# Kernel optimization log

Hardware: AMD Instinct MI355X
Metric: run time of the kernel (lower is better)

The kernel has to match this reference:

```python
import jax, jax.numpy as jnp
import numpy as np


def setup_inputs() -> dict:
    key = jax.random.key(0)
    k1, k2, k3 = jax.random.split(key, 3)
    b_n, f_num, N = 2, 4, 50
    n = b_n * f_num
    C_in, C = 256, 64
    h, w = 200, 336
    return {
        "x": jax.random.normal(k1, (n, C, h * w), jnp.float32),
        "idx_feat": jax.random.normal(k2, (n, C_in, N, 1), jnp.float32),
        "weight": jax.random.normal(k3, (C, C_in), jnp.float32) * 0.01,
        "bias": jnp.zeros((C,), jnp.float32),
        "thing_gt_idx": jnp.ones((b_n, N, f_num), jnp.int32),
        "h": h,
        "w": w,
    }


def _con_loss(mw, b_n, N, f_num, C):
    # mw: (b_n*f_num, C, N, 1) kernel embeddings after embed_extractor
    K = N * f_num
    # reshape/permute mirrors torch: (b_n, N, f_num, C) flattened row-major ->
    # rows ordered (instance, frame), matching the boolean-mask gather order
    # under a dense (all-ones) thing_gt_idx mask.
    m = mw.reshape(b_n, f_num, C, N).transpose(0, 3, 1, 2).reshape(b_n, K, C)
    # F.normalize(dim=1)
    m = m / jnp.maximum(jnp.linalg.norm(m, axis=-1, keepdims=True), 1e-12)
    sim = jnp.einsum('bkc,blc->bkl', m, m)  # (b_n, K, K)
    labels = np.repeat(np.arange(N), f_num)  # instance id per row (static)
    f_own = np.tile(np.arange(f_num), N)     # frame id per row (static)
    # static negative gather indices: all columns of other instances, padded by
    # repeating the last negative (torch's while-loop torch.cat) to length K-1
    neg_cols = []
    for i in range(N):
        cols = np.nonzero(labels != i)[0]
        neg_cols.append(np.concatenate([cols, np.full(f_num - 1, cols[-1])]))
    neg_idx = np.stack(neg_cols)[labels]     # (K, K-1)
    # random positive among the f_num-1 same-instance / other-frame entries
    r = jax.random.randint(jax.random.key(42), (b_n, K), 0, f_num - 1)
    pos_off = jnp.where(r >= f_own[None, :], r + 1, r)
    pos_col = labels[None, :] * f_num + pos_off  # (b_n, K)
    positives = sim[jnp.arange(b_n)[:, None], jnp.arange(K)[None, :], pos_col]
    negatives = sim[:, np.arange(K)[:, None], neg_idx]  # (b_n, K, K-1)
    logits = jnp.concatenate([positives[..., None], negatives], axis=-1) / 0.07
    # CrossEntropyLoss with target 0, mean over K rows, summed over batches
    lse = jax.scipy.special.logsumexp(logits, axis=-1)
    return jnp.sum(jnp.mean(lse - logits[..., 0], axis=-1))


def reference(x, idx_feat, weight, bias, thing_gt_idx, h, w):
    b_n, N, f_num = thing_gt_idx.shape
    n = b_n * f_num
    C = weight.shape[0]
    # embed_extractor: 1x1 conv == channel matmul
    mw = jnp.einsum('bcnk,dc->bdnk', idx_feat, weight) + bias[None, :, None, None]
    loss = _con_loss(mw, b_n, N, f_num, C)
    # shuffle_times == 1 branch: kernels @ encoded features
    kernels = mw.reshape(n, C, N).transpose(0, 2, 1)  # (n, N, C)
    inst_pred = jnp.matmul(kernels, x).reshape(n, N, h, w)
    return inst_pred, loss
```

## Files before the change

kernel.cpp:

```cpp
#include <hip/hip_runtime.h>
#include <stdint.h>
#include <float.h>
#include <math.h>

#define HW_TOT 67200
#define NBF 8
#define CO 64
#define CI 256
#define NN 50
#define KK 200
#define BN 2

__device__ __forceinline__ uint32_t rotl32(uint32_t v, int n) {
  return (v << n) | (v >> (32 - n));
}

__device__ void tf2x32(uint32_t k0, uint32_t k1, uint32_t x0, uint32_t x1,
                       uint32_t& o0, uint32_t& o1) {
  const uint32_t ks2 = k0 ^ k1 ^ 0x1BD11BDAu;
  x0 += k0; x1 += k1;
  x0 += x1; x1 = rotl32(x1, 13); x1 ^= x0;
  x0 += x1; x1 = rotl32(x1, 15); x1 ^= x0;
  x0 += x1; x1 = rotl32(x1, 26); x1 ^= x0;
  x0 += x1; x1 = rotl32(x1, 6);  x1 ^= x0;
  x0 += k1; x1 += ks2 + 1u;
  x0 += x1; x1 = rotl32(x1, 17); x1 ^= x0;
  x0 += x1; x1 = rotl32(x1, 29); x1 ^= x0;
  x0 += x1; x1 = rotl32(x1, 16); x1 ^= x0;
  x0 += x1; x1 = rotl32(x1, 24); x1 ^= x0;
  x0 += ks2; x1 += k0 + 2u;
  x0 += x1; x1 = rotl32(x1, 13); x1 ^= x0;
  x0 += x1; x1 = rotl32(x1, 15); x1 ^= x0;
  x0 += x1; x1 = rotl32(x1, 26); x1 ^= x0;
  x0 += x1; x1 = rotl32(x1, 6);  x1 ^= x0;
  x0 += k0; x1 += k1 + 3u;
  x0 += x1; x1 = rotl32(x1, 17); x1 ^= x0;
  x0 += x1; x1 = rotl32(x1, 29); x1 ^= x0;
  x0 += x1; x1 = rotl32(x1, 16); x1 ^= x0;
  x0 += x1; x1 = rotl32(x1, 24); x1 ^= x0;
  x0 += k1; x1 += ks2 + 4u;
  x0 += x1; x1 = rotl32(x1, 13); x1 ^= x0;
  x0 += x1; x1 = rotl32(x1, 15); x1 ^= x0;
  x0 += x1; x1 = rotl32(x1, 26); x1 ^= x0;
  x0 += x1; x1 = rotl32(x1, 6);  x1 ^= x0;
  o0 = x0 + ks2;
  o1 = x1 + k0 + 5u;
}

__device__ int jax_r(int b, int k) {
  uint32_t k1a, k1b, k2a, k2b, h0, h1, l0, l1;
  tf2x32(0u, 42u, 0u, 0u, k1a, k1b);
  tf2x32(0u, 42u, 0u, 1u, k2a, k2b);
  const uint32_t idx = (uint32_t)(b * KK + k);
  tf2x32(k1a, k1b, 0u, idx, h0, h1);
  tf2x32(k2a, k2b, 0u, idx, l0, l1);
  const uint32_t hb = h0 ^ h1, lb = l0 ^ l1;
  return (int)(((hb % 3u) + (lb % 3u)) % 3u);
}

__global__ __launch_bounds__(256) void k_mw(const float* __restrict__ idx_feat,
                                            const float* __restrict__ weight,
                                            const float* __restrict__ bias,
                                            float* __restrict__ mw) {
  const int tid = blockIdx.x * 256 + threadIdx.x;
  if (tid >= NBF * CO * NN) return;
  const int n = tid % NN;
  const int rest = tid / NN;
  const int d = rest % CO;
  const int b = rest / CO;
  float acc = bias[d];
  const float* feat = idx_feat + (size_t)(b * CI) * NN + n;
  const float* wrow = weight + d * CI;
  #pragma unroll 8
  for (int ci = 0; ci < CI; ++ci)
    acc = fmaf(feat[ci * NN], wrow[ci], acc);
  mw[tid] = acc;
}

__device__ __forceinline__ float waveMax(float v) {
  #pragma unroll
  for (int o = 32; o > 0; o >>= 1) v = fmaxf(v, __shfl_down(v, o));
  return v;
}
__device__ __forceinline__ float waveSum(float v) {
  #pragma unroll
  for (int o = 32; o > 0; o >>= 1) v += __shfl_down(v, o);
  return v;
}

__global__ __launch_bounds__(256) void k_loss(const float* __restrict__ mw,
                                              float* __restrict__ partial) {
  __shared__ __align__(16) float m_lds[KK][68];
  __shared__ float red[8];
  __shared__ float pos_sh;
  __shared__ int rvals[32];

  const int b = blockIdx.x >> 3;
  const int chunk = blockIdx.x & 7;
  const int t = threadIdx.x;
  const int wid = t >> 6, lane = t & 63;
  const int kbase = chunk * 25;

  if (t < 25) rvals[t] = jax_r(b, kbase + t);

  float row[CO];
  if (t < KK) {
    const int f = t & 3, ni = t >> 2;
    const float* src = mw + (size_t)((b * 4 + f) * CO) * NN + ni;
    float ssq = 0.f;
    #pragma unroll
    for (int c = 0; c < CO; ++c) { const float v = src[c * NN]; row[c] = v; ssq += v * v; }
    const float inv = 1.0f / fmaxf(sqrtf(ssq), 1e-12f);
    #pragma unroll
    for (int c = 0; c < CO; ++c) { row[c] *= inv; m_lds[t][c] = row[c]; }
  }
  __syncthreads();

  float part = 0.f;
  for (int kk = 0; kk < 25; ++kk) {
    const int k = kbase + kk;
    const int g = k >> 2, fo = k & 3;
    const int r = rvals[kk];
    const int pos_off = (r >= fo) ? r + 1 : r;
    const int pos_col = (g << 2) + pos_off;
    const int last_neg = (g == NN - 1) ? (KK - 5) : (KK - 1);

    float dot = 0.f;
    if (t < KK) {
      const float4* mk = reinterpret_cast<const float4*>(&m_lds[k][0]);
      #pragma unroll
      for (int c4 = 0; c4 < 16; ++c4) {
        const float4 a = mk[c4];
        dot = fmaf(a.x, row[4 * c4 + 0], dot);
        dot = fmaf(a.y, row[4 * c4 + 1], dot);
        dot = fmaf(a.z, row[4 * c4 + 2], dot);
        dot = fmaf(a.w, row[4 * c4 + 3], dot);
      }
    }
    const float logit = dot * (1.0f / 0.07f);

    float wgt = 0.f;
    if (t < KK) {
      if (t == pos_col) wgt = 1.f;
      else if ((t >> 2) != g) wgt = (t == last_neg) ? 4.f : 1.f;
    }
    const bool valid = wgt > 0.f;

    const float wmax = waveMax(valid ? logit : -FLT_MAX);
    if (lane == 0) red[wid] = wmax;
    if (t == pos_col) pos_sh = logit;
    __syncthreads();
    const float mx = fmaxf(fmaxf(red[0], red[1]), fmaxf(red[2], red[3]));
    const float pos = pos_sh;
    const float ws = waveSum(valid ? wgt * expf(logit - mx) : 0.f);
    if (lane == 0) red[4 + wid] = ws;
    __syncthreads();
    if (t == 0) {
      const float s = red[4] + red[5] + red[6] + red[7];
      part += (mx + logf(s)) - pos;
    }
    __syncthreads();
  }
  if (t == 0) partial[blockIdx.x] = part;
}

typedef __attribute__((ext_vector_type(8))) short bf16x8;
typedef __attribute__((ext_vector_type(4))) float f32x4;

__device__ __forceinline__ uint32_t bf16rne(float f) {
  uint32_t u = __builtin_bit_cast(uint32_t, f);
  return (u + 0x7FFFu + ((u >> 16) & 1u)) >> 16;
}

__global__ __launch_bounds__(256, 4) void k_pred(const float* __restrict__ x,
                                                 const float* __restrict__ mw,
                                                 const float* __restrict__ partial,
                                                 float* __restrict__ out) {
  __shared__ __align__(16) char lds[64 * 128];

  const int b = blockIdx.y;
  const int p0 = blockIdx.x * 64;
  const int u = threadIdx.x;
  const int l = u & 63;
  const int w = u >> 6;
  const int ln = l & 15, lg = l >> 4;

  const float* xb  = x  + (size_t)b * CO * HW_TOT;
  const float* mwb = mw + (size_t)b * CO * NN;

  const int sc0 = 4 * (u >> 4);
  const int sp0 = 4 * (u & 15);
  const float4 v0 = *reinterpret_cast<const float4*>(xb + (size_t)(sc0 + 0) * HW_TOT + p0 + sp0);
  const float4 v1 = *reinterpret_cast<const float4*>(xb + (size_t)(sc0 + 1) * HW_TOT + p0 + sp0);
  const float4 v2 = *reinterpret_cast<const float4*>(xb + (size_t)(sc0 + 2) * HW_TOT + p0 + sp0);
  const float4 v3 = *reinterpret_cast<const float4*>(xb + (size_t)(sc0 + 3) * HW_TOT + p0 + sp0);

  bf16x8 afr[2];
  #pragma unroll
  for (int ks = 0; ks < 2; ++ks) {
    #pragma unroll
    for (int j = 0; j < 8; ++j) {
      const int c = ks * 32 + lg * 8 + j;
      const int n = min(16 * w + ln, NN - 1);
      afr[ks][j] = (short)bf16rne(mwb[c * NN + n]);
    }
  }

  {
    const float c0s[4] = {v0.x, v1.x, v2.x, v3.x};
    const float c1s[4] = {v0.y, v1.y, v2.y, v3.y};
    const float c2s[4] = {v0.z, v1.z, v2.z, v3.z};
    const float c3s[4] = {v0.w, v1.w, v2.w, v3.w};
    const float* cols[4] = {c0s, c1s, c2s, c3s};
    #pragma unroll
    for (int s = 0; s < 4; ++s) {
      const float* cv = cols[s];
      const uint32_t lo = bf16rne(cv[0]) | (bf16rne(cv[1]) << 16);
      const uint32_t hi = bf16rne(cv[2]) | (bf16rne(cv[3]) << 16);
      const int row = sp0 + s;
      const int wb = (row * 128 + sc0 * 2) ^ ((row & 7) << 4);
      *reinterpret_cast<uint2*>(lds + wb) = make_uint2(lo, hi);
    }
  }
  __syncthreads();

  f32x4 acc[4];
  #pragma unroll
  for (int q = 0; q < 4; ++q) acc[q] = (f32x4){0.f, 0.f, 0.f, 0.f};

  #pragma unroll
  for (int ks = 0; ks < 2; ++ks) {
    #pragma unroll
    for (int q = 0; q < 4; ++q) {
      const int row = q * 16 + ln;
      const int rb = (row * 128 + ks * 64 + lg * 16) ^ ((ln & 7) << 4);
      const uint4 raw = *reinterpret_cast<const uint4*>(lds + rb);
      const bf16x8 bfr = __builtin_bit_cast(bf16x8, raw);
      acc[q] = __builtin_amdgcn_mfma_f32_16x16x32_bf16(afr[ks], bfr, acc[q], 0, 0, 0);
    }
  }

  float* ob = out + (size_t)b * NN * HW_TOT + p0;
  #pragma unroll
  for (int q = 0; q < 4; ++q) {
    #pragma unroll
    for (int i = 0; i < 4; ++i) {
      const int n = 16 * w + 4 * lg + i;
      if (n < NN)
        __builtin_nontemporal_store(acc[q][i], ob + (size_t)n * HW_TOT + q * 16 + ln);
    }
  }

  if (blockIdx.x == 0 && b == 0 && u == 0) {
    float s = 0.f;
    #pragma unroll
    for (int i = 0; i < 16; ++i) s += partial[i];
    out[(size_t)NBF * NN * HW_TOT] = s * (1.0f / KK);
  }
}

extern "C" void kernel_launch(void* const* d_in, const int* in_sizes, int n_in,
                              void* d_out, int out_size, void* d_ws, size_t ws_size,
                              hipStream_t stream) {
  const float* x        = (const float*)d_in[0];
  const float* idx_feat = (const float*)d_in[1];
  const float* weight   = (const float*)d_in[2];
  const float* bias     = (const float*)d_in[3];
  float* out = (float*)d_out;

  float* mw = (float*)d_ws;
  float* partial = mw + NBF * CO * NN;

  hipLaunchKernelGGL(k_mw, dim3((NBF * CO * NN + 255) / 256), dim3(256), 0, stream,
                     idx_feat, weight, bias, mw);
  hipLaunchKernelGGL(k_loss, dim3(16), dim3(256), 0, stream, mw, partial);
  hipLaunchKernelGGL(k_pred, dim3(HW_TOT / 64, NBF), dim3(256), 0, stream,
                     x, mw, partial, out);
}
```

Baseline: 92.49 us.

## Process multiple pixel tiles per block with register prefetch of next tile

```diff
diff --git a/kernel.cpp b/kernel.cpp
--- a/kernel.cpp
+++ b/kernel.cpp
@@ -10,6 +10,7 @@
 #define NN 50
 #define KK 200
 #define BN 2
+#define TILES 5
 
 __device__ __forceinline__ uint32_t rotl32(uint32_t v, int n) {
   return (v << n) | (v >> (32 - n));
@@ -179,7 +180,6 @@
   __shared__ __align__(16) char lds[64 * 128];
 
   const int b = blockIdx.y;
-  const int p0 = blockIdx.x * 64;
   const int u = threadIdx.x;
   const int l = u & 63;
   const int w = u >> 6;
@@ -190,10 +190,7 @@
 
   const int sc0 = 4 * (u >> 4);
   const int sp0 = 4 * (u & 15);
-  const float4 v0 = *reinterpret_cast<const float4*>(xb + (size_t)(sc0 + 0) * HW_TOT + p0 + sp0);
-  const float4 v1 = *reinterpret_cast<const float4*>(xb + (size_t)(sc0 + 1) * HW_TOT + p0 + sp0);
-  const float4 v2 = *reinterpret_cast<const float4*>(xb + (size_t)(sc0 + 2) * HW_TOT + p0 + sp0);
-  const float4 v3 = *reinterpret_cast<const float4*>(xb + (size_t)(sc0 + 3) * HW_TOT + p0 + sp0);
+  const int pbase = blockIdx.x * (64 * TILES);
 
   bf16x8 afr[2];
   #pragma unroll
@@ -206,48 +203,71 @@
     }
   }
 
+  float4 v0, v1, v2, v3;
   {
-    const float c0s[4] = {v0.x, v1.x, v2.x, v3.x};
-    const float c1s[4] = {v0.y, v1.y, v2.y, v3.y};
-    const float c2s[4] = {v0.z, v1.z, v2.z, v3.z};
-    const float c3s[4] = {v0.w, v1.w, v2.w, v3.w};
-    const float* cols[4] = {c0s, c1s, c2s, c3s};
-    #pragma unroll
-    for (int s = 0; s < 4; ++s) {
-      const float* cv = cols[s];
-      const uint32_t lo = bf16rne(cv[0]) | (bf16rne(cv[1]) << 16);
-      const uint32_t hi = bf16rne(cv[2]) | (bf16rne(cv[3]) << 16);
-      const int row = sp0 + s;
-      const int wb = (row * 128 + sc0 * 2) ^ ((row & 7) << 4);
-      *reinterpret_cast<uint2*>(lds + wb) = make_uint2(lo, hi);
-    }
-  }
-  __syncthreads();
-
-  f32x4 acc[4];
-  #pragma unroll
-  for (int q = 0; q < 4; ++q) acc[q] = (f32x4){0.f, 0.f, 0.f, 0.f};
-
-  #pragma unroll
-  for (int ks = 0; ks < 2; ++ks) {
-    #pragma unroll
-    for (int q = 0; q < 4; ++q) {
-      const int row = q * 16 + ln;
-      const int rb = (row * 128 + ks * 64 + lg * 16) ^ ((ln & 7) << 4);
-      const uint4 raw = *reinterpret_cast<const uint4*>(lds + rb);
-      const bf16x8 bfr = __builtin_bit_cast(bf16x8, raw);
-      acc[q] = __builtin_amdgcn_mfma_f32_16x16x32_bf16(afr[ks], bfr, acc[q], 0, 0, 0);
-    }
-  }
-
-  float* ob = out + (size_t)b * NN * HW_TOT + p0;
-  #pragma unroll
-  for (int q = 0; q < 4; ++q) {
+    const float* src = xb + (size_t)sc0 * HW_TOT + pbase + sp0;
+    v0 = *reinterpret_cast<const float4*>(src);
+    v1 = *reinterpret_cast<const float4*>(src + HW_TOT);
+    v2 = *reinterpret_cast<const float4*>(src + 2 * (size_t)HW_TOT);
+    v3 = *reinterpret_cast<const float4*>(src + 3 * (size_t)HW_TOT);
+  }
+
+  #pragma unroll 1
+  for (int t = 0; t < TILES; ++t) {
+    if (t > 0) __syncthreads();
+
+    {
+      const float c0s[4] = {v0.x, v1.x, v2.x, v3.x};
+      const float c1s[4] = {v0.y, v1.y, v2.y, v3.y};
+      const float c2s[4] = {v0.z, v1.z, v2.z, v3.z};
+      const float c3s[4] = {v0.w, v1.w, v2.w, v3.w};
+      const float* cols[4] = {c0s, c1s, c2s, c3s};
+      #pragma unroll
+      for (int s = 0; s < 4; ++s) {
+        const float* cv = cols[s];
+        const uint32_t lo = bf16rne(cv[0]) | (bf16rne(cv[1]) << 16);
+        const uint32_t hi = bf16rne(cv[2]) | (bf16rne(cv[3]) << 16);
+        const int row = sp0 + s;
+        const int wb = (row * 128 + sc0 * 2) ^ ((row & 7) << 4);
+        *reinterpret_cast<uint2*>(lds + wb) = make_uint2(lo, hi);
+      }
+    }
+    __syncthreads();
+
+    if (t + 1 < TILES) {
+      const float* src = xb + (size_t)sc0 * HW_TOT + pbase + (t + 1) * 64 + sp0;
+      v0 = *reinterpret_cast<const float4*>(src);
+      v1 = *reinterpret_cast<const float4*>(src + HW_TOT);
+      v2 = *reinterpret_cast<const float4*>(src + 2 * (size_t)HW_TOT);
+      v3 = *reinterpret_cast<const float4*>(src + 3 * (size_t)HW_TOT);
+    }
+
+    f32x4 acc[4];
+    #pragma unroll
+    for (int q = 0; q < 4; ++q) acc[q] = (f32x4){0.f, 0.f, 0.f, 0.f};
+
+    #pragma unroll
+    for (int ks = 0; ks < 2; ++ks) {
+      #pragma unroll
+      for (int q = 0; q < 4; ++q) {
+        const int row = q * 16 + ln;
+        const int rb = (row * 128 + ks * 64 + lg * 16) ^ ((ln & 7) << 4);
+        const uint4 raw = *reinterpret_cast<const uint4*>(lds + rb);
+        const bf16x8 bfr = __builtin_bit_cast(bf16x8, raw);
+        acc[q] = __builtin_amdgcn_mfma_f32_16x16x32_bf16(afr[ks], bfr, acc[q], 0, 0, 0);
+      }
+    }
+
+    float* ob = out + (size_t)b * NN * HW_TOT + pbase + t * 64;
     #pragma unroll
     for (int i = 0; i < 4; ++i) {
       const int n = 16 * w + 4 * lg + i;
-      if (n < NN)
-        __builtin_nontemporal_store(acc[q][i], ob + (size_t)n * HW_TOT + q * 16 + ln);
+      if (n < NN) {
+        float* orow = ob + (size_t)n * HW_TOT + ln;
+        #pragma unroll
+        for (int q = 0; q < 4; ++q)
+          orow[q * 16] = acc[q][i];
+      }
     }
   }
 
@@ -274,6 +294,6 @@
   hipLaunchKernelGGL(k_mw, dim3((NBF * CO * NN + 255) / 256), dim3(256), 0, stream,
                      idx_feat, weight, bias, mw);
   hipLaunchKernelGGL(k_loss, dim3(16), dim3(256), 0, stream, mw, partial);
-  hipLaunchKernelGGL(k_pred, dim3(HW_TOT / 64, NBF), dim3(256), 0, stream,
+  hipLaunchKernelGGL(k_pred, dim3(HW_TOT / (64 * TILES), NBF), dim3(256), 0, stream,
                      x, mw, partial, out);
 }
```

Result: faster. 88.00 us (-4.8%).

## Enlarge pixel tile to 320 with chunked channel staging in LDS

Applied to the files above, without the earlier changes.

```diff
diff --git a/kernel.cpp b/kernel.cpp
--- a/kernel.cpp
+++ b/kernel.cpp
@@ -10,6 +10,8 @@
 #define NN 50
 #define KK 200
 #define BN 2
+#define PT 320
+#define CHK 32
 
 __device__ __forceinline__ uint32_t rotl32(uint32_t v, int n) {
   return (v << n) | (v >> (32 - n));
@@ -172,14 +174,14 @@
   return (u + 0x7FFFu + ((u >> 16) & 1u)) >> 16;
 }
 
-__global__ __launch_bounds__(256, 4) void k_pred(const float* __restrict__ x,
+__global__ __launch_bounds__(256, 3) void k_pred(const float* __restrict__ x,
                                                  const float* __restrict__ mw,
                                                  const float* __restrict__ partial,
                                                  float* __restrict__ out) {
-  __shared__ __align__(16) char lds[64 * 128];
+  __shared__ __align__(16) unsigned short xl[CHK][PT];
 
   const int b = blockIdx.y;
-  const int p0 = blockIdx.x * 64;
+  const int p0 = blockIdx.x * PT;
   const int u = threadIdx.x;
   const int l = u & 63;
   const int w = u >> 6;
@@ -188,13 +190,6 @@
   const float* xb  = x  + (size_t)b * CO * HW_TOT;
   const float* mwb = mw + (size_t)b * CO * NN;
 
-  const int sc0 = 4 * (u >> 4);
-  const int sp0 = 4 * (u & 15);
-  const float4 v0 = *reinterpret_cast<const float4*>(xb + (size_t)(sc0 + 0) * HW_TOT + p0 + sp0);
-  const float4 v1 = *reinterpret_cast<const float4*>(xb + (size_t)(sc0 + 1) * HW_TOT + p0 + sp0);
-  const float4 v2 = *reinterpret_cast<const float4*>(xb + (size_t)(sc0 + 2) * HW_TOT + p0 + sp0);
-  const float4 v3 = *reinterpret_cast<const float4*>(xb + (size_t)(sc0 + 3) * HW_TOT + p0 + sp0);
-
   bf16x8 afr[2];
   #pragma unroll
   for (int ks = 0; ks < 2; ++ks) {
@@ -206,48 +201,73 @@
     }
   }
 
-  {
-    const float c0s[4] = {v0.x, v1.x, v2.x, v3.x};
-    const float c1s[4] = {v0.y, v1.y, v2.y, v3.y};
-    const float c2s[4] = {v0.z, v1.z, v2.z, v3.z};
-    const float c3s[4] = {v0.w, v1.w, v2.w, v3.w};
-    const float* cols[4] = {c0s, c1s, c2s, c3s};
-    #pragma unroll
-    for (int s = 0; s < 4; ++s) {
-      const float* cv = cols[s];
-      const uint32_t lo = bf16rne(cv[0]) | (bf16rne(cv[1]) << 16);
-      const uint32_t hi = bf16rne(cv[2]) | (bf16rne(cv[3]) << 16);
-      const int row = sp0 + s;
-      const int wb = (row * 128 + sc0 * 2) ^ ((row & 7) << 4);
-      *reinterpret_cast<uint2*>(lds + wb) = make_uint2(lo, hi);
-    }
-  }
-  __syncthreads();
-
-  f32x4 acc[4];
-  #pragma unroll
-  for (int q = 0; q < 4; ++q) acc[q] = (f32x4){0.f, 0.f, 0.f, 0.f};
-
-  #pragma unroll
+  f32x4 acc[PT / 16];
+
+  #pragma unroll 1
   for (int ks = 0; ks < 2; ++ks) {
-    #pragma unroll
-    for (int q = 0; q < 4; ++q) {
-      const int row = q * 16 + ln;
-      const int rb = (row * 128 + ks * 64 + lg * 16) ^ ((ln & 7) << 4);
-      const uint4 raw = *reinterpret_cast<const uint4*>(lds + rb);
-      const bf16x8 bfr = __builtin_bit_cast(bf16x8, raw);
+    if (ks > 0) __syncthreads();
+
+    {
+      const int rbase = ks * CHK + w * 8;
+      float4 va[8];
+      #pragma unroll
+      for (int rr = 0; rr < 8; ++rr)
+        va[rr] = *reinterpret_cast<const float4*>(
+            xb + (size_t)(rbase + rr) * HW_TOT + p0 + 4 * l);
+      float4 vt[8];
+      if (l < 16) {
+        #pragma unroll
+        for (int rr = 0; rr < 8; ++rr)
+          vt[rr] = *reinterpret_cast<const float4*>(
+              xb + (size_t)(rbase + rr) * HW_TOT + p0 + 256 + 4 * l);
+      }
+      #pragma unroll
+      for (int rr = 0; rr < 8; ++rr) {
+        ushort4 s;
+        s.x = (unsigned short)bf16rne(va[rr].x);
+        s.y = (unsigned short)bf16rne(va[rr].y);
+        s.z = (unsigned short)bf16rne(va[rr].z);
+        s.w = (unsigned short)bf16rne(va[rr].w);
+        *reinterpret_cast<ushort4*>(&xl[w * 8 + rr][4 * l]) = s;
+      }
+      if (l < 16) {
+        #pragma unroll
+        for (int rr = 0; rr < 8; ++rr) {
+          ushort4 s;
+          s.x = (unsigned short)bf16rne(vt[rr].x);
+          s.y = (unsigned short)bf16rne(vt[rr].y);
+          s.z = (unsigned short)bf16rne(vt[rr].z);
+          s.w = (unsigned short)bf16rne(vt[rr].w);
+          *reinterpret_cast<ushort4*>(&xl[w * 8 + rr][256 + 4 * l]) = s;
+        }
+      }
+    }
+    __syncthreads();
+
+    if (ks == 0) {
+      #pragma unroll
+      for (int q = 0; q < PT / 16; ++q) acc[q] = (f32x4){0.f, 0.f, 0.f, 0.f};
+    }
+
+    #pragma unroll
+    for (int q = 0; q < PT / 16; ++q) {
+      bf16x8 bfr;
+      #pragma unroll
+      for (int j = 0; j < 8; ++j)
+        bfr[j] = (short)xl[lg * 8 + j][q * 16 + ln];
       acc[q] = __builtin_amdgcn_mfma_f32_16x16x32_bf16(afr[ks], bfr, acc[q], 0, 0, 0);
     }
   }
 
   float* ob = out + (size_t)b * NN * HW_TOT + p0;
   #pragma unroll
-  for (int q = 0; q < 4; ++q) {
-    #pragma unroll
-    for (int i = 0; i < 4; ++i) {
-      const int n = 16 * w + 4 * lg + i;
-      if (n < NN)
-        __builtin_nontemporal_store(acc[q][i], ob + (size_t)n * HW_TOT + q * 16 + ln);
+  for (int i = 0; i < 4; ++i) {
+    const int n = 16 * w + 4 * lg + i;
+    if (n < NN) {
+      float* orow = ob + (size_t)n * HW_TOT + ln;
+      #pragma unroll
+      for (int q = 0; q < PT / 16; ++q)
+        orow[q * 16] = acc[q][i];
     }
   }
 
@@ -274,6 +294,6 @@
   hipLaunchKernelGGL(k_mw, dim3((NBF * CO * NN + 255) / 256), dim3(256), 0, stream,
                      idx_feat, weight, bias, mw);
   hipLaunchKernelGGL(k_loss, dim3(16), dim3(256), 0, stream, mw, partial);
-  hipLaunchKernelGGL(k_pred, dim3(HW_TOT / 64, NBF), dim3(256), 0, stream,
+  hipLaunchKernelGGL(k_pred, dim3(HW_TOT / PT, NBF), dim3(256), 0, stream,
                      x, mw, partial, out);
 }
```

Result: no change. 93.90 us (+1.5%).
